# Kernel tuning notes

Hardware: AMD Instinct MI355X
Metric: run time of the kernel (lower is better)

The kernel has to match this reference:

```python
import itertools
import jax, jax.numpy as jnp
import numpy as np

N1 = 4
N2 = 4
D = 3
BATCH = 512
NDENSE = 256
FEAT_IN = (N1 + N2) * D  # 24


def _perms_and_signs(n):
    P = np.array(list(itertools.permutations(range(n))), dtype=np.int32)  # [n!, n], lexicographic
    # sign = (-1)^(number of inversions)
    triu = np.triu(np.ones((n, n), dtype=np.int64), 1)
    inv = np.sum((P[:, :, None] > P[:, None, :]) * triu, axis=(1, 2))
    signs = np.where(inv % 2 == 0, 1.0, -1.0).astype(np.float32)
    return P, signs

P1_np, S1_np = _perms_and_signs(N1)
P2_np, S2_np = _perms_and_signs(N2)


def setup_inputs() -> dict:
    key = jax.random.key(0)
    ks = jax.random.split(key, 12)
    def dense_init(k, fan_in, fan_out):
        return jax.random.normal(k, (fan_in, fan_out), jnp.float32) / jnp.sqrt(jnp.float32(fan_in))
    inp = {
        "x1": jax.random.normal(ks[0], (BATCH, N1, D), jnp.float32),
        "x2": jax.random.normal(ks[1], (BATCH, N2, D), jnp.float32),
        "W0": dense_init(ks[2], FEAT_IN, NDENSE),
        "b0": jnp.zeros((NDENSE,), jnp.float32),
        "W1": dense_init(ks[3], NDENSE, NDENSE),
        "b1": jnp.zeros((NDENSE,), jnp.float32),
        "W2": dense_init(ks[4], NDENSE, NDENSE),
        "b2": jnp.zeros((NDENSE,), jnp.float32),
        "Wf": dense_init(ks[5], NDENSE, 1),
        "bf": jnp.zeros((1,), jnp.float32),
    }
    return inp


def _resnet(h, W0, b0, W1, b1, W2, b2, Wf, bf):
    # SimpleResNet: residual tanh dense layers (skip when shapes match), linear head
    y = jnp.tanh(h @ W0 + b0)            # [.., 24] -> [.., 256]: no skip (shape mismatch)
    y = jnp.tanh(y @ W1 + b1) + y        # residual
    y = jnp.tanh(y @ W2 + b2) + y        # residual
    return y @ Wf + bf                   # [.., 1], no activation


def reference(x1, x2, W0, b0, W1, b1, W2, b2, Wf, bf):
    P1 = jnp.asarray(P1_np); P2 = jnp.asarray(P2_np)
    s1 = jnp.asarray(S1_np); s2 = jnp.asarray(S2_np)
    nf1, nf2 = P1.shape[0], P2.shape[0]  # 24, 24
    # all permutations along particle axis
    p1 = jnp.take(x1, P1, axis=-2)       # [B, nf1, n1, d]
    p2 = jnp.take(x2, P2, axis=-2)       # [B, nf2, n2, d]
    # broadcast to cross product of permutation axes
    b1_ = jnp.broadcast_to(p1[:, :, None, :, :], (x1.shape[0], nf1, nf2, N1, D))
    b2_ = jnp.broadcast_to(p2[:, None, :, :, :], (x2.shape[0], nf1, nf2, N2, D))
    concat = jnp.concatenate([b1_, b2_], axis=-2)                  # [B, nf1, nf2, n1+n2, d]
    feats = concat.reshape(concat.shape[:-2] + (-1,))              # [B, nf1, nf2, (n1+n2)*d]
    out = _resnet(feats, W0, b0, W1, b1, W2, b2, Wf, bf)           # [B, nf1, nf2, 1]
    signed = out * s1[:, None, None] * s2[:, None]                 # sign-weighted
    anti = jnp.sum(signed, axis=(-1, -2, -3))                      # [B]
    return jnp.log(jnp.abs(anti))
```

## Files before the change

### kernel.cpp

```cpp
#include <hip/hip_runtime.h>
#include <math.h>

#define ND 256
#define RPB 32
#define RPW 8
#define ROWS_PER_B 576
#define BATCH 512
#define NBLOCKS (BATCH * ROWS_PER_B / RPB)
#define YSTR 264

__constant__ int c_P[24 * 4] = {
    0,1,2,3, 0,1,3,2, 0,2,1,3, 0,2,3,1, 0,3,1,2, 0,3,2,1,
    1,0,2,3, 1,0,3,2, 1,2,0,3, 1,2,3,0, 1,3,0,2, 1,3,2,0,
    2,0,1,3, 2,0,3,1, 2,1,0,3, 2,1,3,0, 2,3,0,1, 2,3,1,0,
    3,0,1,2, 3,0,2,1, 3,1,0,2, 3,1,2,0, 3,2,0,1, 3,2,1,0
};
__constant__ float c_S[24] = {
     1.f,-1.f,-1.f, 1.f, 1.f,-1.f,
    -1.f, 1.f, 1.f,-1.f,-1.f, 1.f,
     1.f,-1.f,-1.f, 1.f, 1.f,-1.f,
    -1.f, 1.f, 1.f,-1.f,-1.f, 1.f
};

__global__ __launch_bounds__(256, 2)
void fused_resnet(const float* __restrict__ x1, const float* __restrict__ x2,
                  const float* __restrict__ W0, const float* __restrict__ b0,
                  const float* __restrict__ W1, const float* __restrict__ b1,
                  const float* __restrict__ W2, const float* __restrict__ b2,
                  const float* __restrict__ Wf, const float* __restrict__ bf,
                  double* __restrict__ anti)
{
    __shared__ __align__(16) float smem[13568];
    float* sW  = smem;
    float* sY  = smem + 4096;
    float* sF  = smem + 12544;
    float* sWf = smem + 13312;

    const int t    = threadIdx.x;
    const int lane = t & 63;
    const int wv   = t >> 6;
    const int r0   = wv * RPW;
    const int gr0  = blockIdx.x * RPB;
    const int b    = gr0 / ROWS_PER_B;

    for (int i = t; i < RPB * 24; i += 256) {
        int lr = i / 24, c = i % 24;
        int pp = (gr0 + lr) % ROWS_PER_B;
        float v;
        if (c < 12) {
            v = x1[b * 12 + c_P[(pp / 24) * 4 + c / 3] * 3 + (c % 3)];
        } else {
            int cc = c - 12;
            v = x2[b * 12 + c_P[(pp % 24) * 4 + cc / 3] * 3 + (cc % 3)];
        }
        sF[i] = v;
    }
    {
        const float4* src = (const float4*)W0;
        float4* dst = (float4*)sY;
        #pragma unroll
        for (int i = 0; i < 6; ++i) dst[t + 256 * i] = src[t + 256 * i];
    }
    if (t < 64) ((float4*)sWf)[t] = ((const float4*)Wf)[t];
    __syncthreads();

    float acc[RPW][4];
    float y[RPW][4];

    #pragma unroll
    for (int r = 0; r < RPW; ++r) { acc[r][0]=0.f; acc[r][1]=0.f; acc[r][2]=0.f; acc[r][3]=0.f; }
    #pragma unroll 1
    for (int k4 = 0; k4 < 6; ++k4) {
        const float4* wp = (const float4*)&sY[(k4 * 4) * ND] + lane;
        float4 w0 = wp[0], w1 = wp[64], w2 = wp[128], w3 = wp[192];
        #pragma unroll
        for (int r = 0; r < RPW; ++r) {
            float4 yv = *(const float4*)&sF[(r0 + r) * 24 + k4 * 4];
            acc[r][0] = fmaf(yv.x, w0.x, acc[r][0]);
            acc[r][1] = fmaf(yv.x, w0.y, acc[r][1]);
            acc[r][2] = fmaf(yv.x, w0.z, acc[r][2]);
            acc[r][3] = fmaf(yv.x, w0.w, acc[r][3]);
            acc[r][0] = fmaf(yv.y, w1.x, acc[r][0]);
            acc[r][1] = fmaf(yv.y, w1.y, acc[r][1]);
            acc[r][2] = fmaf(yv.y, w1.z, acc[r][2]);
            acc[r][3] = fmaf(yv.y, w1.w, acc[r][3]);
            acc[r][0] = fmaf(yv.z, w2.x, acc[r][0]);
            acc[r][1] = fmaf(yv.z, w2.y, acc[r][1]);
            acc[r][2] = fmaf(yv.z, w2.z, acc[r][2]);
            acc[r][3] = fmaf(yv.z, w2.w, acc[r][3]);
            acc[r][0] = fmaf(yv.w, w3.x, acc[r][0]);
            acc[r][1] = fmaf(yv.w, w3.y, acc[r][1]);
            acc[r][2] = fmaf(yv.w, w3.z, acc[r][2]);
            acc[r][3] = fmaf(yv.w, w3.w, acc[r][3]);
        }
    }
    __syncthreads();
    {
        float4 bv = *(const float4*)&b0[4 * lane];
        #pragma unroll
        for (int r = 0; r < RPW; ++r) {
            y[r][0] = tanhf(acc[r][0] + bv.x);
            y[r][1] = tanhf(acc[r][1] + bv.y);
            y[r][2] = tanhf(acc[r][2] + bv.z);
            y[r][3] = tanhf(acc[r][3] + bv.w);
            float4 o; o.x = y[r][0]; o.y = y[r][1]; o.z = y[r][2]; o.w = y[r][3];
            *(float4*)&sY[(r0 + r) * YSTR + 4 * lane] = o;
        }
    }

    #pragma unroll 1
    for (int L = 0; L < 2; ++L) {
        const float* __restrict__ Wg = L ? W2 : W1;
        const float* __restrict__ bp = L ? b2 : b1;
        #pragma unroll
        for (int r = 0; r < RPW; ++r) { acc[r][0]=0.f; acc[r][1]=0.f; acc[r][2]=0.f; acc[r][3]=0.f; }
        #pragma unroll 1
        for (int T = 0; T < 16; ++T) {
            __syncthreads();
            {
                const float4* src = (const float4*)(Wg + T * 16 * ND);
                float4* dst = (float4*)sW;
                #pragma unroll
                for (int i = 0; i < 4; ++i) dst[t + 256 * i] = src[t + 256 * i];
            }
            __syncthreads();
            #pragma unroll
            for (int q = 0; q < 4; ++q) {
                const float4* wp = (const float4*)&sW[(q * 4) * ND] + lane;
                float4 w0 = wp[0], w1 = wp[64], w2 = wp[128], w3 = wp[192];
                const int kt = T * 16 + q * 4;
                #pragma unroll
                for (int r = 0; r < RPW; ++r) {
                    float4 yv = *(const float4*)&sY[(r0 + r) * YSTR + kt];
                    acc[r][0] = fmaf(yv.x, w0.x, acc[r][0]);
                    acc[r][1] = fmaf(yv.x, w0.y, acc[r][1]);
                    acc[r][2] = fmaf(yv.x, w0.z, acc[r][2]);
                    acc[r][3] = fmaf(yv.x, w0.w, acc[r][3]);
                    acc[r][0] = fmaf(yv.y, w1.x, acc[r][0]);
                    acc[r][1] = fmaf(yv.y, w1.y, acc[r][1]);
                    acc[r][2] = fmaf(yv.y, w1.z, acc[r][2]);
                    acc[r][3] = fmaf(yv.y, w1.w, acc[r][3]);
                    acc[r][0] = fmaf(yv.z, w2.x, acc[r][0]);
                    acc[r][1] = fmaf(yv.z, w2.y, acc[r][1]);
                    acc[r][2] = fmaf(yv.z, w2.z, acc[r][2]);
                    acc[r][3] = fmaf(yv.z, w2.w, acc[r][3]);
                    acc[r][0] = fmaf(yv.w, w3.x, acc[r][0]);
                    acc[r][1] = fmaf(yv.w, w3.y, acc[r][1]);
                    acc[r][2] = fmaf(yv.w, w3.z, acc[r][2]);
                    acc[r][3] = fmaf(yv.w, w3.w, acc[r][3]);
                }
            }
        }
        float4 bv = *(const float4*)&bp[4 * lane];
        #pragma unroll
        for (int r = 0; r < RPW; ++r) {
            y[r][0] = tanhf(acc[r][0] + bv.x) + y[r][0];
            y[r][1] = tanhf(acc[r][1] + bv.y) + y[r][1];
            y[r][2] = tanhf(acc[r][2] + bv.z) + y[r][2];
            y[r][3] = tanhf(acc[r][3] + bv.w) + y[r][3];
            float4 o; o.x = y[r][0]; o.y = y[r][1]; o.z = y[r][2]; o.w = y[r][3];
            *(float4*)&sY[(r0 + r) * YSTR + 4 * lane] = o;
        }
    }

    __syncthreads();
    double contrib = 0.0;
    if (t < RPB) {
        const float* yrow = &sY[t * YSTR];
        float f = 0.f;
        #pragma unroll 8
        for (int k = 0; k < ND; ++k) f = fmaf(yrow[k], sWf[k], f);
        f += bf[0];
        int pp = (gr0 + t) % ROWS_PER_B;
        contrib = (double)(c_S[pp / 24] * c_S[pp % 24]) * (double)f;
    }
    if (wv == 0) {
        #pragma unroll
        for (int off = 32; off > 0; off >>= 1) contrib += __shfl_xor(contrib, off, 64);
        if (lane == 0) atomicAdd(&anti[b], contrib);
    }
}

__global__ void finalize_log(const double* __restrict__ anti, float* __restrict__ out) {
    int i = blockIdx.x * 256 + threadIdx.x;
    if (i < BATCH) out[i] = (float)log(fabs(anti[i]));
}

extern "C" void kernel_launch(void* const* d_in, const int* in_sizes, int n_in,
                              void* d_out, int out_size, void* d_ws, size_t ws_size,
                              hipStream_t stream) {
    const float* x1 = (const float*)d_in[0];
    const float* x2 = (const float*)d_in[1];
    const float* W0 = (const float*)d_in[2];
    const float* b0 = (const float*)d_in[3];
    const float* W1 = (const float*)d_in[4];
    const float* b1 = (const float*)d_in[5];
    const float* W2 = (const float*)d_in[6];
    const float* b2 = (const float*)d_in[7];
    const float* Wf = (const float*)d_in[8];
    const float* bf = (const float*)d_in[9];
    double* anti = (double*)d_ws;
    float* out   = (float*)d_out;

    (void)hipMemsetAsync(anti, 0, BATCH * sizeof(double), stream);
    fused_resnet<<<NBLOCKS, 256, 0, stream>>>(x1, x2, W0, b0, W1, b1, W2, b2, Wf, bf, anti);
    finalize_log<<<(BATCH + 255) / 256, 256, 0, stream>>>(anti, out);
}
```

Before: 1.259 ms.

## Stream weights from global/L1 into registers, drop shared weight staging, raise occupancy

Removes the shared-memory staging of W0/W1/W2 and the block-wide barriers around each tile. Each wave now loads weight float4s straight from global (L1/L2-cached) into registers, with a two-stage software prefetch. The residual y array is dropped from registers and reread from shared memory. The smaller LDS footprint and the launch bound raised to 4 blocks per CU are meant to increase occupancy and cut sync overhead. The risks are more global/L1 traffic, since every wave refetches the weights, and register pressure from the prefetch buffers.

```diff
diff --git a/kernel.cpp b/kernel.cpp
--- a/kernel.cpp
+++ b/kernel.cpp
@@ -7,7 +7,7 @@
 #define ROWS_PER_B 576
 #define BATCH 512
 #define NBLOCKS (BATCH * ROWS_PER_B / RPB)
-#define YSTR 264
+#define YSTR 260
 
 __constant__ int c_P[24 * 4] = {
     0,1,2,3, 0,1,3,2, 0,2,1,3, 0,2,3,1, 0,3,1,2, 0,3,2,1,
@@ -22,7 +22,7 @@
     -1.f, 1.f, 1.f,-1.f,-1.f, 1.f
 };
 
-__global__ __launch_bounds__(256, 2)
+__global__ __launch_bounds__(256, 4)
 void fused_resnet(const float* __restrict__ x1, const float* __restrict__ x2,
                   const float* __restrict__ W0, const float* __restrict__ b0,
                   const float* __restrict__ W1, const float* __restrict__ b1,
@@ -30,11 +30,10 @@
                   const float* __restrict__ Wf, const float* __restrict__ bf,
                   double* __restrict__ anti)
 {
-    __shared__ __align__(16) float smem[13568];
-    float* sW  = smem;
-    float* sY  = smem + 4096;
-    float* sF  = smem + 12544;
-    float* sWf = smem + 13312;
+    __shared__ __align__(16) float smem[9344];
+    float* sF  = smem;
+    float* sWf = smem + 768;
+    float* sY  = smem + 1024;
 
     const int t    = threadIdx.x;
     const int lane = t & 63;
@@ -55,27 +54,20 @@
         }
         sF[i] = v;
     }
-    {
-        const float4* src = (const float4*)W0;
-        float4* dst = (float4*)sY;
-        #pragma unroll
-        for (int i = 0; i < 6; ++i) dst[t + 256 * i] = src[t + 256 * i];
-    }
     if (t < 64) ((float4*)sWf)[t] = ((const float4*)Wf)[t];
     __syncthreads();
 
     float acc[RPW][4];
-    float y[RPW][4];
 
     #pragma unroll
     for (int r = 0; r < RPW; ++r) { acc[r][0]=0.f; acc[r][1]=0.f; acc[r][2]=0.f; acc[r][3]=0.f; }
     #pragma unroll 1
-    for (int k4 = 0; k4 < 6; ++k4) {
-        const float4* wp = (const float4*)&sY[(k4 * 4) * ND] + lane;
-        float4 w0 = wp[0], w1 = wp[64], w2 = wp[128], w3 = wp[192];
+    for (int j = 0; j < 6; ++j) {
+        const float4* p = (const float4*)W0 + j * 256 + lane;
+        float4 w0 = p[0], w1 = p[64], w2 = p[128], w3 = p[192];
         #pragma unroll
         for (int r = 0; r < RPW; ++r) {
-            float4 yv = *(const float4*)&sF[(r0 + r) * 24 + k4 * 4];
+            float4 yv = *(const float4*)&sF[(r0 + r) * 24 + j * 4];
             acc[r][0] = fmaf(yv.x, w0.x, acc[r][0]);
             acc[r][1] = fmaf(yv.x, w0.y, acc[r][1]);
             acc[r][2] = fmaf(yv.x, w0.z, acc[r][2]);
@@ -94,16 +86,15 @@
             acc[r][3] = fmaf(yv.w, w3.w, acc[r][3]);
         }
     }
-    __syncthreads();
     {
         float4 bv = *(const float4*)&b0[4 * lane];
         #pragma unroll
         for (int r = 0; r < RPW; ++r) {
-            y[r][0] = tanhf(acc[r][0] + bv.x);
-            y[r][1] = tanhf(acc[r][1] + bv.y);
-            y[r][2] = tanhf(acc[r][2] + bv.z);
-            y[r][3] = tanhf(acc[r][3] + bv.w);
-            float4 o; o.x = y[r][0]; o.y = y[r][1]; o.z = y[r][2]; o.w = y[r][3];
+            float4 o;
+            o.x = tanhf(acc[r][0] + bv.x);
+            o.y = tanhf(acc[r][1] + bv.y);
+            o.z = tanhf(acc[r][2] + bv.z);
+            o.w = tanhf(acc[r][3] + bv.w);
             *(float4*)&sY[(r0 + r) * YSTR + 4 * lane] = o;
         }
     }
@@ -112,53 +103,72 @@
     for (int L = 0; L < 2; ++L) {
         const float* __restrict__ Wg = L ? W2 : W1;
         const float* __restrict__ bp = L ? b2 : b1;
+        const float4* pw = (const float4*)Wg + lane;
         #pragma unroll
         for (int r = 0; r < RPW; ++r) { acc[r][0]=0.f; acc[r][1]=0.f; acc[r][2]=0.f; acc[r][3]=0.f; }
+
+        float4 wA0 = pw[0], wA1 = pw[64], wA2 = pw[128], wA3 = pw[192];
+        float4 wB0, wB1, wB2, wB3;
         #pragma unroll 1
-        for (int T = 0; T < 16; ++T) {
-            __syncthreads();
+        for (int j = 0; j < 64; j += 2) {
             {
-                const float4* src = (const float4*)(Wg + T * 16 * ND);
-                float4* dst = (float4*)sW;
-                #pragma unroll
-                for (int i = 0; i < 4; ++i) dst[t + 256 * i] = src[t + 256 * i];
-            }
-            __syncthreads();
+                const float4* p = pw + (j + 1) * 256;
+                wB0 = p[0]; wB1 = p[64]; wB2 = p[128]; wB3 = p[192];
+            }
             #pragma unroll
-            for (int q = 0; q < 4; ++q) {
-                const float4* wp = (const float4*)&sW[(q * 4) * ND] + lane;
-                float4 w0 = wp[0], w1 = wp[64], w2 = wp[128], w3 = wp[192];
-                const int kt = T * 16 + q * 4;
-                #pragma unroll
-                for (int r = 0; r < RPW; ++r) {
-                    float4 yv = *(const float4*)&sY[(r0 + r) * YSTR + kt];
-                    acc[r][0] = fmaf(yv.x, w0.x, acc[r][0]);
-                    acc[r][1] = fmaf(yv.x, w0.y, acc[r][1]);
-                    acc[r][2] = fmaf(yv.x, w0.z, acc[r][2]);
-                    acc[r][3] = fmaf(yv.x, w0.w, acc[r][3]);
-                    acc[r][0] = fmaf(yv.y, w1.x, acc[r][0]);
-                    acc[r][1] = fmaf(yv.y, w1.y, acc[r][1]);
-                    acc[r][2] = fmaf(yv.y, w1.z, acc[r][2]);
-                    acc[r][3] = fmaf(yv.y, w1.w, acc[r][3]);
-                    acc[r][0] = fmaf(yv.z, w2.x, acc[r][0]);
-                    acc[r][1] = fmaf(yv.z, w2.y, acc[r][1]);
-                    acc[r][2] = fmaf(yv.z, w2.z, acc[r][2]);
-                    acc[r][3] = fmaf(yv.z, w2.w, acc[r][3]);
-                    acc[r][0] = fmaf(yv.w, w3.x, acc[r][0]);
-                    acc[r][1] = fmaf(yv.w, w3.y, acc[r][1]);
-                    acc[r][2] = fmaf(yv.w, w3.z, acc[r][2]);
-                    acc[r][3] = fmaf(yv.w, w3.w, acc[r][3]);
-                }
+            for (int r = 0; r < RPW; ++r) {
+                float4 yv = *(const float4*)&sY[(r0 + r) * YSTR + j * 4];
+                acc[r][0] = fmaf(yv.x, wA0.x, acc[r][0]);
+                acc[r][1] = fmaf(yv.x, wA0.y, acc[r][1]);
+                acc[r][2] = fmaf(yv.x, wA0.z, acc[r][2]);
+                acc[r][3] = fmaf(yv.x, wA0.w, acc[r][3]);
+                acc[r][0] = fmaf(yv.y, wA1.x, acc[r][0]);
+                acc[r][1] = fmaf(yv.y, wA1.y, acc[r][1]);
+                acc[r][2] = fmaf(yv.y, wA1.z, acc[r][2]);
+                acc[r][3] = fmaf(yv.y, wA1.w, acc[r][3]);
+                acc[r][0] = fmaf(yv.z, wA2.x, acc[r][0]);
+                acc[r][1] = fmaf(yv.z, wA2.y, acc[r][1]);
+                acc[r][2] = fmaf(yv.z, wA2.z, acc[r][2]);
+                acc[r][3] = fmaf(yv.z, wA2.w, acc[r][3]);
+                acc[r][0] = fmaf(yv.w, wA3.x, acc[r][0]);
+                acc[r][1] = fmaf(yv.w, wA3.y, acc[r][1]);
+                acc[r][2] = fmaf(yv.w, wA3.z, acc[r][2]);
+                acc[r][3] = fmaf(yv.w, wA3.w, acc[r][3]);
+            }
+            if (j + 2 < 64) {
+                const float4* p = pw + (j + 2) * 256;
+                wA0 = p[0]; wA1 = p[64]; wA2 = p[128]; wA3 = p[192];
+            }
+            #pragma unroll
+            for (int r = 0; r < RPW; ++r) {
+                float4 yv = *(const float4*)&sY[(r0 + r) * YSTR + j * 4 + 4];
+                acc[r][0] = fmaf(yv.x, wB0.x, acc[r][0]);
+                acc[r][1] = fmaf(yv.x, wB0.y, acc[r][1]);
+                acc[r][2] = fmaf(yv.x, wB0.z, acc[r][2]);
+                acc[r][3] = fmaf(yv.x, wB0.w, acc[r][3]);
+                acc[r][0] = fmaf(yv.y, wB1.x, acc[r][0]);
+                acc[r][1] = fmaf(yv.y, wB1.y, acc[r][1]);
+                acc[r][2] = fmaf(yv.y, wB1.z, acc[r][2]);
+                acc[r][3] = fmaf(yv.y, wB1.w, acc[r][3]);
+                acc[r][0] = fmaf(yv.z, wB2.x, acc[r][0]);
+                acc[r][1] = fmaf(yv.z, wB2.y, acc[r][1]);
+                acc[r][2] = fmaf(yv.z, wB2.z, acc[r][2]);
+                acc[r][3] = fmaf(yv.z, wB2.w, acc[r][3]);
+                acc[r][0] = fmaf(yv.w, wB3.x, acc[r][0]);
+                acc[r][1] = fmaf(yv.w, wB3.y, acc[r][1]);
+                acc[r][2] = fmaf(yv.w, wB3.z, acc[r][2]);
+                acc[r][3] = fmaf(yv.w, wB3.w, acc[r][3]);
             }
         }
         float4 bv = *(const float4*)&bp[4 * lane];
         #pragma unroll
         for (int r = 0; r < RPW; ++r) {
-            y[r][0] = tanhf(acc[r][0] + bv.x) + y[r][0];
-            y[r][1] = tanhf(acc[r][1] + bv.y) + y[r][1];
-            y[r][2] = tanhf(acc[r][2] + bv.z) + y[r][2];
-            y[r][3] = tanhf(acc[r][3] + bv.w) + y[r][3];
-            float4 o; o.x = y[r][0]; o.y = y[r][1]; o.z = y[r][2]; o.w = y[r][3];
+            float4 yo = *(const float4*)&sY[(r0 + r) * YSTR + 4 * lane];
+            float4 o;
+            o.x = tanhf(acc[r][0] + bv.x) + yo.x;
+            o.y = tanhf(acc[r][1] + bv.y) + yo.y;
+            o.z = tanhf(acc[r][2] + bv.z) + yo.z;
+            o.w = tanhf(acc[r][3] + bv.w) + yo.w;
             *(float4*)&sY[(r0 + r) * YSTR + 4 * lane] = o;
         }
     }
```

Measured after the change: 1.241 ms. No clear change (-1.4%).
